# Performance work log

Hardware: AMD Instinct MI355X
Metric: run time of the kernel (lower is better)

## Reference

```python
import jax, jax.numpy as jnp
import numpy as np

N, IN_DIM, OUT_DIM, HEADS = 4096, 256, 256, 8
D_HEAD = (OUT_DIM * HEADS) // HEADS  # = OUT_DIM per the torch code
HIDDEN = OUT_DIM * 4
LN_EPS = 1e-5


def setup_inputs() -> dict:
    key = jax.random.key(0)
    ks = jax.random.split(key, 8)
    s = 0.02
    return {
        "x": jax.random.normal(ks[0], (N, IN_DIM), jnp.float32),
        "Wq": jax.random.normal(ks[1], (OUT_DIM * HEADS, IN_DIM), jnp.float32) * s,
        "Wk": jax.random.normal(ks[2], (OUT_DIM * HEADS, IN_DIM), jnp.float32) * s,
        "Wv": jax.random.normal(ks[3], (OUT_DIM * HEADS, IN_DIM), jnp.float32) * s,
        "Wo": jax.random.normal(ks[4], (OUT_DIM, OUT_DIM * HEADS), jnp.float32) * s,
        "bo": jnp.zeros((OUT_DIM,), jnp.float32),
        "ln1_g": jnp.ones((IN_DIM,), jnp.float32),
        "ln1_b": jnp.zeros((IN_DIM,), jnp.float32),
        "ln2_g": jnp.ones((OUT_DIM,), jnp.float32),
        "ln2_b": jnp.zeros((OUT_DIM,), jnp.float32),
        "W1": jax.random.normal(ks[5], (HIDDEN, OUT_DIM), jnp.float32) * s,
        "b1": jnp.zeros((HIDDEN,), jnp.float32),
        "W2": jax.random.normal(ks[6], (OUT_DIM, HIDDEN), jnp.float32) * s,
        "b2": jnp.zeros((OUT_DIM,), jnp.float32),
    }


def _layernorm(x, g, b):
    mu = jnp.mean(x, axis=-1, keepdims=True)
    var = jnp.mean(jnp.square(x - mu), axis=-1, keepdims=True)
    return (x - mu) * jax.lax.rsqrt(var + LN_EPS) * g + b


def reference(x, Wq, Wk, Wv, Wo, bo, ln1_g, ln1_b, ln2_g, ln2_b, W1, b1, W2, b2):
    n = x.shape[0]
    h = _layernorm(x, ln1_g, ln1_b)
    # projections: F.linear(h, W) = h @ W.T, viewed as [N, H, d_head]
    Q = (h @ Wq.T).reshape(n, HEADS, D_HEAD)
    K = (h @ Wk.T).reshape(n, HEADS, D_HEAD)
    V = (h @ Wv.T).reshape(n, HEADS, D_HEAD)
    scores = jnp.einsum('nhd,mhd->nhm', Q, K) / jnp.sqrt(jnp.float32(D_HEAD))
    probs = jax.nn.softmax(scores, axis=-1)
    attn = jnp.einsum('nhm,mhd->nhd', probs, V).reshape(n, HEADS * D_HEAD)
    attn_out = attn @ Wo.T + bo
    x = x + attn_out  # proj_residual is Identity (in_dim == out_dim)
    h2 = _layernorm(x, ln2_g, ln2_b)
    ffn = jax.nn.gelu(h2 @ W1.T + b1, approximate=False) @ W2.T + b2
    return x + ffn
```

## Files before the change

kernel.cpp:

```cpp
#include <hip/hip_runtime.h>

typedef __attribute__((ext_vector_type(8))) short short8;
typedef __attribute__((ext_vector_type(4))) float f32x4;
typedef __attribute__((ext_vector_type(16))) float f32x16;
typedef __attribute__((ext_vector_type(8))) int i32x8;
typedef unsigned short u16;
typedef unsigned int u32;
typedef unsigned char u8;

#define DEVFN static __device__ __forceinline__

DEVFN u16 f2b(float f) {
  u32 u = __builtin_bit_cast(u32, f);
  u32 r = u + 0x7fffu + ((u >> 16) & 1u);
  return (u16)(r >> 16);
}

DEVFN float b2f(u16 b) {
  u32 u = ((u32)b) << 16;
  return __builtin_bit_cast(float, u);
}

DEVFN short8 ldfrag(const void* p) {
  return __builtin_bit_cast(short8, *(const uint4*)p);
}

#define MFMA16(a, b, c) __builtin_amdgcn_mfma_f32_16x16x32_bf16((a), (b), (c), 0, 0, 0)
#define MFMAS(a, b, c) __builtin_amdgcn_mfma_scale_f32_32x32x64_f8f6f4((a), (b), (c), 0, 0, 0, 127, 0, 127)
#define MFMASW(a, b, c) __builtin_amdgcn_mfma_scale_f32_32x32x64_f8f6f4((a), (b), (c), 0, 0, 0, 127, 0, 123)
#define EXP2(x) __builtin_amdgcn_exp2f(x)
#define CVT8(a, b, o, hi) __builtin_amdgcn_cvt_pk_fp8_f32((a), (b), (o), (hi))

DEVFN i32x8 mk8(uint4 a, uint4 b) {
  return (i32x8){(int)a.x, (int)a.y, (int)a.z, (int)a.w, (int)b.x, (int)b.y, (int)b.z, (int)b.w};
}

DEVFN void llds16(const void* g, void* l) {
  __builtin_amdgcn_global_load_lds((const __attribute__((address_space(1))) void*)g,
                                   (__attribute__((address_space(3))) void*)l, 16, 0, 0);
}

DEVFN float gelu_exact(float v) {
  return 0.5f * v * (1.0f + erff(v * 0.70710678118654752f));
}

DEVFN int sigma(int d) {
  return (d & ~24) | ((d & 8) << 1) | ((d & 16) >> 1);
}

DEVFN size_t c8off(int row, int k) {
  return (size_t)(row >> 5) * 8192 + (k >> 6) * 2048 + ((row & 31) + 32 * ((k >> 5) & 1)) * 32 + (k & 31);
}

__global__ __launch_bounds__(256) void k_prep(const float* Wq, const float* Wk, const float* Wv,
                                              const float* Wo, const float* W1, const float* W2,
                                              u8* Wq8, u8* Wk8, u8* Wv8,
                                              u16* Wob, u8* W18, u16* W2b,
                                              const float* x, const float* g1, const float* be1,
                                              u8* h8c) {
  const int y = blockIdx.y;
  if (y < 3) {
    int i = blockIdx.x * 256 + threadIdx.x;
    if (i >= 131072) return;
    const float* s = y == 0 ? Wq : (y == 1 ? Wk : Wv);
    u8* d = y == 0 ? Wq8 : (y == 1 ? Wk8 : Wv8);
    float4 v = ((const float4*)s)[i];
    const int col = i >> 6, k = (i & 63) * 4;
    u32 q = CVT8(v.x * 16.0f, v.y * 16.0f, 0, false);
    q = CVT8(v.z * 16.0f, v.w * 16.0f, q, true);
    *(u32*)(d + c8off(col, k)) = q;
    return;
  }
  if (y == 4) {
    int i = blockIdx.x * 256 + threadIdx.x;
    if (i >= 65536) return;
    float4 v = ((const float4*)W1)[i];
    const int col = i >> 6, k = (i & 63) * 4;
    u32 q = CVT8(v.x * 16.0f, v.y * 16.0f, 0, false);
    q = CVT8(v.z * 16.0f, v.w * 16.0f, q, true);
    *(u32*)(W18 + c8off(col, k)) = q;
    return;
  }
  if (y < 6) {
    int i = blockIdx.x * 256 + threadIdx.x;
    const float* s = (y == 3) ? Wo : W2;
    u16* d = (y == 3) ? Wob : W2b;
    int n4 = (y == 3) ? 131072 : 65536;
    if (i >= n4) return;
    float4 v = ((const float4*)s)[i];
    ushort4 o = { f2b(v.x), f2b(v.y), f2b(v.z), f2b(v.w) };
    ((ushort4*)d)[i] = o;
    return;
  }
  int row = blockIdx.x * 4 + (threadIdx.x >> 6);
  int l = threadIdx.x & 63;
  const float4 v = *(const float4*)(x + (size_t)row * 256 + l * 4);
  float s = v.x + v.y + v.z + v.w;
#pragma unroll
  for (int m = 1; m < 64; m <<= 1) s += __shfl_xor(s, m);
  float mu = s * (1.0f / 256.0f);
  float dx = v.x - mu, dy = v.y - mu, dz = v.z - mu, dw = v.w - mu;
  float q = dx * dx + dy * dy + dz * dz + dw * dw;
#pragma unroll
  for (int m = 1; m < 64; m <<= 1) q += __shfl_xor(q, m);
  float r = rsqrtf(q * (1.0f / 256.0f) + 1e-5f);
  float4 gv = *(const float4*)(g1 + l * 4);
  float4 bv = *(const float4*)(be1 + l * 4);
  u32 pk = CVT8(dx * r * gv.x + bv.x, dy * r * gv.y + bv.y, 0, false);
  pk = CVT8(dz * r * gv.z + bv.z, dw * r * gv.w + bv.w, pk, true);
  *(u32*)(h8c + c8off(row, l * 4)) = pk;
}

__global__ __launch_bounds__(256, 2) void k_gemm_sk(const u16* __restrict__ A,
                                                    const u16* __restrict__ B,
                                                    u16* __restrict__ out,
                                                    int M, int N, int K) {
  __shared__ __attribute__((aligned(16))) u16 As[128 * 32];
  __shared__ __attribute__((aligned(16))) u16 Bs[128 * 32];
  const int t = threadIdx.x;
  const int w = t >> 6, l = t & 63, g = l >> 4, c = l & 15;
  const int wr = w >> 1, wc = w & 1;
  const int bm = blockIdx.y, bn = blockIdx.x;

  f32x4 acc[4][4] = {};
  int nk = (K >> 5) / gridDim.z, kk0 = blockIdx.z * nk;

  const int srow = t >> 2;
  const int sj = t & 3;
  const char* Abase = (const char*)A;
  const char* Bbase = (const char*)B;

  for (int kk = kk0; kk < kk0 + nk; ++kk) {
    const size_t kb = (size_t)kk * 64;
    uint4 a0 = *(const uint4*)(Abase + ((size_t)(bm * 128 + srow) * K) * 2 + kb + sj * 16);
    uint4 a1 = *(const uint4*)(Abase + ((size_t)(bm * 128 + srow + 64) * K) * 2 + kb + sj * 16);
    uint4 b0 = *(const uint4*)(Bbase + ((size_t)(bn * 128 + srow) * K) * 2 + kb + sj * 16);
    uint4 b1 = *(const uint4*)(Bbase + ((size_t)(bn * 128 + srow + 64) * K) * 2 + kb + sj * 16);
    __syncthreads();
    const int sw0 = (sj * 16) ^ (((srow >> 1) & 3) << 4);
    const int sw1 = (sj * 16) ^ ((((srow + 64) >> 1) & 3) << 4);
    *(uint4*)((char*)As + srow * 64 + sw0) = a0;
    *(uint4*)((char*)As + (srow + 64) * 64 + sw1) = a1;
    *(uint4*)((char*)Bs + srow * 64 + sw0) = b0;
    *(uint4*)((char*)Bs + (srow + 64) * 64 + sw1) = b1;
    __syncthreads();
    short8 af[4], bfr[4];
#pragma unroll
    for (int m = 0; m < 4; ++m) {
      int row = wr * 64 + m * 16 + c;
      af[m] = ldfrag((const char*)As + row * 64 + ((g * 16) ^ (((row >> 1) & 3) << 4)));
    }
#pragma unroll
    for (int n = 0; n < 4; ++n) {
      int row = wc * 64 + n * 16 + c;
      bfr[n] = ldfrag((const char*)Bs + row * 64 + ((g * 16) ^ (((row >> 1) & 3) << 4)));
    }
#pragma unroll
    for (int m = 0; m < 4; ++m)
#pragma unroll
      for (int n = 0; n < 4; ++n) acc[m][n] = MFMA16(af[m], bfr[n], acc[m][n]);
  }

  const int row0 = bm * 128 + wr * 64 + 4 * g;
  const int col0 = bn * 128 + wc * 64 + c;
  u16* po = out + (size_t)blockIdx.z * M * N;
#pragma unroll
  for (int m = 0; m < 4; ++m)
#pragma unroll
    for (int n = 0; n < 4; ++n)
#pragma unroll
      for (int rr = 0; rr < 4; ++rr)
        po[(size_t)(row0 + m * 16 + rr) * N + col0 + n * 16] = f2b(acc[m][n][rr]);
}

__global__ __launch_bounds__(256, 2) void k_gemm_wo(const u16* __restrict__ part,
                                                    const float* __restrict__ ml,
                                                    const u16* __restrict__ B,
                                                    u16* __restrict__ out) {
  constexpr int M = 4096, N = 256, K = 2048;
  __shared__ __attribute__((aligned(16))) u16 As[128 * 32];
  __shared__ __attribute__((aligned(16))) u16 Bs[128 * 32];
  const int t = threadIdx.x;
  const int w = t >> 6, l = t & 63, g = l >> 4, c = l & 15;
  const int wr = w >> 1, wc = w & 1;
  const int bm = blockIdx.y, bn = blockIdx.x;
  const int nk = 16, kk0 = blockIdx.z * 16;
  const int h0 = kk0 >> 3;

  const int srow = t >> 2;
  const int sj = t & 3;
  const int r0 = bm * 128 + srow, r1 = r0 + 64;

  float wgt[4];
#pragma unroll
  for (int rr = 0; rr < 2; ++rr) {
    const int row = rr ? r1 : r0;
#pragma unroll
    for (int hh = 0; hh < 2; ++hh) {
      const int h = h0 + hh;
      float l0 = ml[(0 + h) * 4096 + row];
      float l1 = ml[(8 + h) * 4096 + row];
      wgt[rr * 2 + hh] = 1.0f / (l0 + l1);
    }
  }

  f32x4 acc[4][4] = {};
  const char* Pbase = (const char*)part;
  const char* Bbase = (const char*)B;
  const size_t PSTRIDE = (size_t)4096 * 2048 * 2;

  for (int kk = kk0; kk < kk0 + nk; ++kk) {
    const int hh = (kk >> 3) & 1;
    const size_t kb = (size_t)kk * 64;
    const size_t a0off = ((size_t)r0 * K) * 2 + kb + sj * 16;
    const size_t a1off = ((size_t)r1 * K) * 2 + kb + sj * 16;
    uint4 p00 = *(const uint4*)(Pbase + a0off);
    uint4 p01 = *(const uint4*)(Pbase + PSTRIDE + a0off);
    uint4 p10 = *(const uint4*)(Pbase + a1off);
    uint4 p11 = *(const uint4*)(Pbase + PSTRIDE + a1off);
    uint4 b0 = *(const uint4*)(Bbase + ((size_t)(bn * 128 + srow) * K) * 2 + kb + sj * 16);
    uint4 b1 = *(const uint4*)(Bbase + ((size_t)(bn * 128 + srow + 64) * K) * 2 + kb + sj * 16);

    float w0 = wgt[hh], w1 = wgt[2 + hh];
    uint4 a0, a1;
    {
      const u16* x0 = (const u16*)&p00;
      const u16* x1 = (const u16*)&p01;
      u16* o = (u16*)&a0;
#pragma unroll
      for (int j = 0; j < 8; ++j) o[j] = f2b((b2f(x0[j]) + b2f(x1[j])) * w0);
      const u16* y0 = (const u16*)&p10;
      const u16* y1 = (const u16*)&p11;
      u16* o1 = (u16*)&a1;
#pragma unroll
      for (int j = 0; j < 8; ++j) o1[j] = f2b((b2f(y0[j]) + b2f(y1[j])) * w1);
    }

    __syncthreads();
    const int sw0 = (sj * 16) ^ (((srow >> 1) & 3) << 4);
    const int sw1 = (sj * 16) ^ ((((srow + 64) >> 1) & 3) << 4);
    *(uint4*)((char*)As + srow * 64 + sw0) = a0;
    *(uint4*)((char*)As + (srow + 64) * 64 + sw1) = a1;
    *(uint4*)((char*)Bs + srow * 64 + sw0) = b0;
    *(uint4*)((char*)Bs + (srow + 64) * 64 + sw1) = b1;
    __syncthreads();
    short8 af[4], bfr[4];
#pragma unroll
    for (int m = 0; m < 4; ++m) {
      int row = wr * 64 + m * 16 + c;
      af[m] = ldfrag((const char*)As + row * 64 + ((g * 16) ^ (((row >> 1) & 3) << 4)));
    }
#pragma unroll
    for (int n = 0; n < 4; ++n) {
      int row = wc * 64 + n * 16 + c;
      bfr[n] = ldfrag((const char*)Bs + row * 64 + ((g * 16) ^ (((row >> 1) & 3) << 4)));
    }
#pragma unroll
    for (int m = 0; m < 4; ++m)
#pragma unroll
      for (int n = 0; n < 4; ++n) acc[m][n] = MFMA16(af[m], bfr[n], acc[m][n]);
  }

  const int row0 = bm * 128 + wr * 64 + 4 * g;
  const int col0 = bn * 128 + wc * 64 + c;
  u16* po = out + (size_t)blockIdx.z * M * N;
#pragma unroll
  for (int m = 0; m < 4; ++m)
#pragma unroll
    for (int n = 0; n < 4; ++n)
#pragma unroll
      for (int rr = 0; rr < 4; ++rr)
        po[(size_t)(row0 + m * 16 + rr) * N + col0 + n * 16] = f2b(acc[m][n][rr]);
}

__global__ __launch_bounds__(256, 2) void k_gemm_qkv(const u8* __restrict__ h8c,
                                                     const u8* __restrict__ Wq8,
                                                     const u8* __restrict__ Wk8,
                                                     const u8* __restrict__ Wv8,
                                                     u8* __restrict__ Oq,
                                                     u8* __restrict__ Ok,
                                                     u8* __restrict__ Ov8) {
  __shared__ __attribute__((aligned(16))) char As[32768];
  __shared__ __attribute__((aligned(16))) char Bs[32768];
  const int t = threadIdx.x;
  const int w = t >> 6, l = t & 63;
  const int q31 = l & 31, hi = l >> 5;
  const int wr = w >> 1, wc = w & 1;
  const int sel = blockIdx.x >> 4;
  const int bn = blockIdx.x & 15;
  const int bm = blockIdx.y;
  const u8* B = sel == 0 ? Wq8 : (sel == 1 ? Wk8 : Wv8);

#pragma unroll
  for (int ii = 0; ii < 8; ++ii) {
    const int inst = w * 8 + ii;
    llds16(h8c + (size_t)bm * 32768 + inst * 1024 + l * 16, As + inst * 1024);
  }
#pragma unroll
  for (int ii = 0; ii < 8; ++ii) {
    const int inst = w * 8 + ii;
    llds16(B + (size_t)bn * 32768 + inst * 1024 + l * 16, Bs + inst * 1024);
  }
  asm volatile("s_waitcnt vmcnt(0)" ::: "memory");
  __builtin_amdgcn_s_barrier();

  f32x16 acc[2][2] = {};
#pragma unroll
  for (int ks = 0; ks < 4; ++ks) {
    i32x8 af[2], bf8[2];
#pragma unroll
    for (int m = 0; m < 2; ++m) {
      const char* p = As + ((wr * 2 + m) * 4 + ks) * 2048 + l * 32;
      af[m] = mk8(*(const uint4*)p, *(const uint4*)(p + 16));
    }
#pragma unroll
    for (int n = 0; n < 2; ++n) {
      const char* p = Bs + ((wc * 2 + n) * 4 + ks) * 2048 + l * 32;
      bf8[n] = mk8(*(const uint4*)p, *(const uint4*)(p + 16));
    }
#pragma unroll
    for (int m = 0; m < 2; ++m)
#pragma unroll
      for (int n = 0; n < 2; ++n) acc[m][n] = MFMASW(af[m], bf8[n], acc[m][n]);
  }

#pragma unroll
  for (int m = 0; m < 2; ++m) {
#pragma unroll
    for (int n = 0; n < 2; ++n) {
      const int col = bn * 128 + wc * 64 + n * 32 + q31;
      const int rbase = bm * 128 + wr * 64 + m * 32 + 4 * hi;
      const int d = col & 255, h = col >> 8;
#pragma unroll
      for (int j = 0; j < 4; ++j) {
        const int kv0 = rbase + 8 * j;
        u32 q = CVT8(acc[m][n][4 * j], acc[m][n][4 * j + 1], 0, false);
        q = CVT8(acc[m][n][4 * j + 2], acc[m][n][4 * j + 3], q, true);
        if (sel == 0) {
#pragma unroll
          for (int e = 0; e < 4; ++e)
            Oq[(size_t)(kv0 + e) * 2048 + col] = (u8)(q >> (8 * e));
        } else if (sel == 1) {
#pragma unroll
          for (int e = 0; e < 4; ++e) {
            const int kv = kv0 + e;
            Ok[(size_t)h * 1048576 + (size_t)(kv >> 5) * 8192 + (d >> 6) * 2048 +
               (((d & 31) >> 4)) * 1024 + ((kv & 31) + 32 * ((d >> 5) & 1)) * 16 + (d & 15)] =
                (u8)(q >> (8 * e));
          }
        } else {
          const int s = sigma(kv0 & 31);
          *(u32*)(Ov8 + (size_t)h * 1048576 + (size_t)(kv0 >> 6) * 16384 + (d >> 5) * 2048 +
                  ((kv0 >> 5) & 1) * 1024 + ((d & 31) + 32 * (s >> 4)) * 16 + (s & 15)) = q;
        }
      }
    }
  }
}

__global__ __launch_bounds__(256, 2) void k_gemm_ffn1(const u8* __restrict__ A8,
                                                      const u8* __restrict__ B8,
                                                      const float* __restrict__ bias,
                                                      u16* __restrict__ out) {
  __shared__ __attribute__((aligned(16))) char As[32768];
  __shared__ __attribute__((aligned(16))) char Bs[32768];
  const int t = threadIdx.x;
  const int w = t >> 6, l = t & 63;
  const int q31 = l & 31, hi = l >> 5;
  const int wr = w >> 1, wc = w & 1;
  const int bn = blockIdx.x;
  const int bm = blockIdx.y;

#pragma unroll
  for (int ii = 0; ii < 8; ++ii) {
    const int inst = w * 8 + ii;
    llds16(A8 + (size_t)bm * 32768 + inst * 1024 + l * 16, As + inst * 1024);
  }
#pragma unroll
  for (int ii = 0; ii < 8; ++ii) {
    const int inst = w * 8 + ii;
    llds16(B8 + (size_t)bn * 32768 + inst * 1024 + l * 16, Bs + inst * 1024);
  }
  asm volatile("s_waitcnt vmcnt(0)" ::: "memory");
  __builtin_amdgcn_s_barrier();

  f32x16 acc[2][2] = {};
#pragma unroll
  for (int ks = 0; ks < 4; ++ks) {
    i32x8 af[2], bf8[2];
#pragma unroll
    for (int m = 0; m < 2; ++m) {
      const char* p = As + ((wr * 2 + m) * 4 + ks) * 2048 + l * 32;
      af[m] = mk8(*(const uint4*)p, *(const uint4*)(p + 16));
    }
#pragma unroll
    for (int n = 0; n < 2; ++n) {
      const char* p = Bs + ((wc * 2 + n) * 4 + ks) * 2048 + l * 32;
      bf8[n] = mk8(*(const uint4*)p, *(const uint4*)(p + 16));
    }
#pragma unroll
    for (int m = 0; m < 2; ++m)
#pragma unroll
      for (int n = 0; n < 2; ++n) acc[m][n] = MFMASW(af[m], bf8[n], acc[m][n]);
  }

#pragma unroll
  for (int m = 0; m < 2; ++m) {
#pragma unroll
    for (int n = 0; n < 2; ++n) {
      const int col = bn * 128 + wc * 64 + n * 32 + q31;
      const int rbase = bm * 128 + wr * 64 + m * 32 + 4 * hi;
      const float bc = bias[col];
#pragma unroll
      for (int j = 0; j < 4; ++j) {
        const int r0j = rbase + 8 * j;
#pragma unroll
        for (int e = 0; e < 4; ++e)
          out[(size_t)(r0j + e) * 1024 + col] = f2b(gelu_exact(acc[m][n][4 * j + e] + bc));
      }
    }
  }
}

__global__ __launch_bounds__(256) void k_red4(const u16* __restrict__ p,
                                              const float* __restrict__ bias,
                                              const float* __restrict__ resid,
                                              float* __restrict__ out) {
  int i = blockIdx.x * 256 + threadIdx.x;
  ushort4 a = *(const ushort4*)(p + (size_t)i * 4);
  ushort4 b = *(const ushort4*)(p + 1048576 * 1 + (size_t)i * 4);
  ushort4 c = *(const ushort4*)(p + 1048576 * 2 + (size_t)i * 4);
  ushort4 d = *(const ushort4*)(p + 1048576 * 3 + (size_t)i * 4);
  float4 r = ((const float4*)resid)[i];
  float4 bb = ((const float4*)bias)[i & 63];
  float4 o;
  o.x = b2f(a.x) + b2f(b.x) + b2f(c.x) + b2f(d.x) + r.x + bb.x;
  o.y = b2f(a.y) + b2f(b.y) + b2f(c.y) + b2f(d.y) + r.y + bb.y;
  o.z = b2f(a.z) + b2f(b.z) + b2f(c.z) + b2f(d.z) + r.z + bb.z;
  o.w = b2f(a.w) + b2f(b.w) + b2f(c.w) + b2f(d.w) + r.w + bb.w;
  ((float4*)out)[i] = o;
}

__global__ __launch_bounds__(256) void k_red4ln(const u16* __restrict__ p,
                                                const float* __restrict__ bias,
                                                const float* __restrict__ resid,
                                                const float* __restrict__ g,
                                                const float* __restrict__ b,
                                                float* __restrict__ x2,
                                                u8* __restrict__ h28) {
  int row = blockIdx.x * 4 + (threadIdx.x >> 6);
  int l = threadIdx.x & 63;
  int i = row * 64 + l;
  ushort4 a = *(const ushort4*)(p + (size_t)i * 4);
  ushort4 bq = *(const ushort4*)(p + 1048576 * 1 + (size_t)i * 4);
  ushort4 cq = *(const ushort4*)(p + 1048576 * 2 + (size_t)i * 4);
  ushort4 dq = *(const ushort4*)(p + 1048576 * 3 + (size_t)i * 4);
  float4 r = ((const float4*)resid)[i];
  float4 bi = ((const float4*)bias)[l];
  float4 v;
  v.x = b2f(a.x) + b2f(bq.x) + b2f(cq.x) + b2f(dq.x) + r.x + bi.x;
  v.y = b2f(a.y) + b2f(bq.y) + b2f(cq.y) + b2f(dq.y) + r.y + bi.y;
  v.z = b2f(a.z) + b2f(bq.z) + b2f(cq.z) + b2f(dq.z) + r.z + bi.z;
  v.w = b2f(a.w) + b2f(bq.w) + b2f(cq.w) + b2f(dq.w) + r.w + bi.w;
  ((float4*)x2)[i] = v;
  float s = v.x + v.y + v.z + v.w;
#pragma unroll
  for (int m = 1; m < 64; m <<= 1) s += __shfl_xor(s, m);
  float mu = s * (1.0f / 256.0f);
  float dx = v.x - mu, dy = v.y - mu, dz = v.z - mu, dw = v.w - mu;
  float q = dx * dx + dy * dy + dz * dz + dw * dw;
#pragma unroll
  for (int m = 1; m < 64; m <<= 1) q += __shfl_xor(q, m);
  float rr = rsqrtf(q * (1.0f / 256.0f) + 1e-5f);
  float4 gv = *(const float4*)(g + l * 4);
  float4 bv = *(const float4*)(b + l * 4);
  u32 pk = CVT8(dx * rr * gv.x + bv.x, dy * rr * gv.y + bv.y, 0, false);
  pk = CVT8(dz * rr * gv.z + bv.z, dw * rr * gv.w + bv.w, pk, true);
  *(u32*)(h28 + c8off(row, l * 4)) = pk;
}

__global__ __launch_bounds__(256, 2) void k_attn(const u8* __restrict__ Q8,
                                                 const u8* __restrict__ K8,
                                                 const u8* __restrict__ V8,
                                                 u16* __restrict__ part,
                                                 float* __restrict__ ml) {
  __shared__ __attribute__((aligned(16))) char smem[49152];
  const int t = threadIdx.x;
  const int w = t >> 6, l = t & 63;
  const int q31 = l & 31, hi = l >> 5;
  const int head = blockIdx.x, qb = blockIdx.y, sp = blockIdx.z;
  const int cbase = sp * 64;
  const float C2 = 0.0625f * 1.44269504f;
  const float MC = 16.0f * C2;

  i32x8 qv[4];
  {
    const u8* qp = Q8 + (size_t)(qb * 128 + w * 32 + q31) * 2048 + head * 256 + hi * 32;
#pragma unroll
    for (int m = 0; m < 4; ++m)
      qv[m] = mk8(*(const uint4*)(qp + m * 64), *(const uint4*)(qp + m * 64 + 16));
  }

  f32x16 o[8] = {};
  float lsum = 0.0f;

  const u8* Kc = K8 + (size_t)head * 1048576;
  const u8* Vc = V8 + (size_t)head * 1048576;

  auto stageK = [&](int cc) {
    char* kd = smem + (cc & 1) * 8192;
    const u8* src = Kc + (size_t)(cbase + cc) * 8192;
#pragma unroll
    for (int ii = 0; ii < 2; ++ii) {
      const int inst = w * 2 + ii;
      llds16(src + inst * 1024 + l * 16, kd + inst * 1024);
    }
  };
  auto stageV = [&](int pp) {
    char* vd = smem + 16384 + (pp & 1) * 16384;
    const u8* src = Vc + (size_t)(sp * 32 + pp) * 16384;
#pragma unroll
    for (int ii = 0; ii < 4; ++ii) {
      const int inst = w * 4 + ii;
      llds16(src + inst * 1024 + l * 16, vd + inst * 1024);
    }
  };

  auto qkchunk = [&](int c, u32 pq[4]) {
    const char* kd = smem + (c & 1) * 8192;
    f32x16 s = {};
    __builtin_amdgcn_s_setprio(1);
#pragma unroll
    for (int m = 0; m < 4; ++m) {
      uint4 k0 = *(const uint4*)(kd + m * 2048 + l * 16);
      uint4 k1 = *(const uint4*)(kd + m * 2048 + 1024 + l * 16);
      s = MFMAS(mk8(k0, k1), qv[m], s);
    }
    __builtin_amdgcn_s_setprio(0);
    float p[16];
#pragma unroll
    for (int i = 0; i < 16; ++i) p[i] = EXP2(fmaf(s[i], C2, -MC));
    float r8[8];
#pragma unroll
    for (int i = 0; i < 8; ++i) r8[i] = p[i] + p[i + 8];
#pragma unroll
    for (int i = 0; i < 4; ++i) r8[i] += r8[i + 4];
    float rs = (r8[0] + r8[1]) + (r8[2] + r8[3]);
    rs += __shfl_xor(rs, 32);
    lsum += rs;
    u32 a0 = CVT8(p[0], p[1], 0, false);
    a0 = CVT8(p[2], p[3], a0, true);
    u32 a1 = CVT8(p[4], p[5], 0, false);
    a1 = CVT8(p[6], p[7], a1, true);
    u32 a2 = CVT8(p[8], p[9], 0, false);
    a2 = CVT8(p[10], p[11], a2, true);
    u32 a3 = CVT8(p[12], p[13], 0, false);
    a3 = CVT8(p[14], p[15], a3, true);
    asm("v_permlane32_swap_b32 %0, %1" : "+v"(a0), "+v"(a1));
    asm("v_permlane32_swap_b32 %0, %1" : "+v"(a2), "+v"(a3));
    pq[0] = a0; pq[1] = a1; pq[2] = a2; pq[3] = a3;
  };

  stageK(0);
  stageV(0);
  for (int cp = 0; cp < 32; ++cp) {
    const int c0 = 2 * cp;
    asm volatile("s_waitcnt vmcnt(4)" ::: "memory");
    __builtin_amdgcn_s_barrier();
    __builtin_amdgcn_sched_barrier(0);
    stageK(c0 + 1);
    u32 pe[4];
    qkchunk(c0, pe);

    asm volatile("s_waitcnt vmcnt(0)" ::: "memory");
    __builtin_amdgcn_s_barrier();
    __builtin_amdgcn_sched_barrier(0);
    if (cp < 31) {
      stageK(c0 + 2);
      stageV(cp + 1);
    }
    u32 po[4];
    qkchunk(c0 + 1, po);

    i32x8 a8 = {(int)pe[0], (int)pe[1], (int)pe[2], (int)pe[3],
                (int)po[0], (int)po[1], (int)po[2], (int)po[3]};
    const char* vd = smem + 16384 + (cp & 1) * 16384;
    __builtin_amdgcn_s_setprio(1);
#pragma unroll
    for (int dt = 0; dt < 8; ++dt) {
      uint4 v0 = *(const uint4*)(vd + dt * 2048 + l * 16);
      uint4 v1 = *(const uint4*)(vd + dt * 2048 + 1024 + l * 16);
      o[dt] = MFMAS(a8, mk8(v0, v1), o[dt]);
    }
    __builtin_amdgcn_s_setprio(0);
  }

  u16* pb = part + (size_t)sp * 4096 * 2048;
#pragma unroll
  for (int i = 0; i < 16; ++i) {
    const int r = (i & 3) + 8 * (i >> 2) + 4 * hi;
    const size_t qg = (size_t)(qb * 128 + w * 32 + r);
#pragma unroll
    for (int dt = 0; dt < 8; ++dt)
      pb[qg * 2048 + head * 256 + dt * 32 + q31] = f2b(o[dt][i]);
  }
  if (hi == 0) {
    const int qg = qb * 128 + w * 32 + q31;
    ml[(sp * 8 + head) * 4096 + qg] = lsum;
  }
}

extern "C" void kernel_launch(void* const* d_in, const int* in_sizes, int n_in,
                              void* d_out, int out_size, void* d_ws, size_t ws_size,
                              hipStream_t stream) {
  const float* x   = (const float*)d_in[0];
  const float* Wq  = (const float*)d_in[1];
  const float* Wk  = (const float*)d_in[2];
  const float* Wv  = (const float*)d_in[3];
  const float* Wo  = (const float*)d_in[4];
  const float* bo  = (const float*)d_in[5];
  const float* g1  = (const float*)d_in[6];
  const float* be1 = (const float*)d_in[7];
  const float* g2  = (const float*)d_in[8];
  const float* be2 = (const float*)d_in[9];
  const float* W1  = (const float*)d_in[10];
  const float* b1  = (const float*)d_in[11];
  const float* W2  = (const float*)d_in[12];
  const float* b2  = (const float*)d_in[13];

  char* ws = (char*)d_ws;
  size_t off = 0;
  auto alloc = [&](size_t n) {
    char* p = ws + off;
    off = (off + n + 255) & ~(size_t)255;
    return p;
  };
  u8*  h8c   = (u8*)alloc(4096 * 256);
  u8*  Wq8   = (u8*)alloc(2048 * 256);
  u8*  Wk8   = (u8*)alloc(2048 * 256);
  u8*  Wv8   = (u8*)alloc(2048 * 256);
  u16* Wob   = (u16*)alloc(256 * 2048 * 2);
  u8*  W18   = (u8*)alloc(1024 * 256);
  u16* W2b   = (u16*)alloc(256 * 1024 * 2);
  u8*  Qb8   = (u8*)alloc((size_t)4096 * 2048);
  u8*  Kb8   = (u8*)alloc((size_t)4096 * 2048);
  u8*  Vb8   = (u8*)alloc((size_t)2048 * 4096);
  u16* attnb = (u16*)alloc((size_t)2 * 4096 * 2048 * 2);
  float* mlb = (float*)alloc(16 * 4096 * 4);
  float* x2  = (float*)alloc(4096 * 256 * 4);
  u8*  h28   = (u8*)alloc(4096 * 256);
  u16* ffn1  = (u16*)alloc((size_t)4096 * 1024 * 2);
  u16* pbuf  = (u16*)Qb8;

  k_prep<<<dim3(1024, 7), 256, 0, stream>>>(Wq, Wk, Wv, Wo, W1, W2,
                                            Wq8, Wk8, Wv8, Wob, W18, W2b,
                                            x, g1, be1, h8c);

  k_gemm_qkv<<<dim3(48, 32), 256, 0, stream>>>(h8c, Wq8, Wk8, Wv8, Qb8, Kb8, Vb8);

  k_attn<<<dim3(8, 32, 2), 256, 0, stream>>>(Qb8, Kb8, Vb8, attnb, mlb);

  k_gemm_wo<<<dim3(2, 32, 4), 256, 0, stream>>>(attnb, mlb, Wob, pbuf);
  k_red4ln<<<1024, 256, 0, stream>>>(pbuf, bo, x, g2, be2, x2, h28);
  k_gemm_ffn1<<<dim3(8, 32), 256, 0, stream>>>(h28, W18, b1, ffn1);
  k_gemm_sk<<<dim3(2, 32, 4), 256, 0, stream>>>(ffn1, W2b, pbuf, 4096, 256, 1024);
  k_red4<<<1024, 256, 0, stream>>>(pbuf, b2, x2, (float*)d_out);
}
```

Measured before the change: 144.9 us.

## Quantize FFN hidden activations and W2 to fp8 and use fp8 MFMA for FFN2

```diff
diff --git a/kernel.cpp b/kernel.cpp
--- a/kernel.cpp
+++ b/kernel.cpp
@@ -51,11 +51,14 @@
 DEVFN size_t c8off(int row, int k) {
   return (size_t)(row >> 5) * 8192 + (k >> 6) * 2048 + ((row & 31) + 32 * ((k >> 5) & 1)) * 32 + (k & 31);
 }
+DEVFN size_t c8off1k(int row, int k) {
+  return (size_t)(row >> 5) * 32768 + (k >> 6) * 2048 + ((row & 31) + 32 * ((k >> 5) & 1)) * 32 + (k & 31);
+}
 
 __global__ __launch_bounds__(256) void k_prep(const float* Wq, const float* Wk, const float* Wv,
                                               const float* Wo, const float* W1, const float* W2,
                                               u8* Wq8, u8* Wk8, u8* Wv8,
-                                              u16* Wob, u8* W18, u16* W2b,
+                                              u16* Wob, u8* W18, u8* W28,
                                               const float* x, const float* g1, const float* be1,
                                               u8* h8c) {
   const int y = blockIdx.y;
@@ -81,15 +84,22 @@
     *(u32*)(W18 + c8off(col, k)) = q;
     return;
   }
-  if (y < 6) {
+  if (y == 5) {
     int i = blockIdx.x * 256 + threadIdx.x;
-    const float* s = (y == 3) ? Wo : W2;
-    u16* d = (y == 3) ? Wob : W2b;
-    int n4 = (y == 3) ? 131072 : 65536;
-    if (i >= n4) return;
-    float4 v = ((const float4*)s)[i];
+    if (i >= 65536) return;
+    float4 v = ((const float4*)W2)[i];
+    const int row = i >> 8, k = (i & 255) * 4;
+    u32 q = CVT8(v.x * 16.0f, v.y * 16.0f, 0, false);
+    q = CVT8(v.z * 16.0f, v.w * 16.0f, q, true);
+    *(u32*)(W28 + c8off1k(row, k)) = q;
+    return;
+  }
+  if (y == 3) {
+    int i = blockIdx.x * 256 + threadIdx.x;
+    if (i >= 131072) return;
+    float4 v = ((const float4*)Wo)[i];
     ushort4 o = { f2b(v.x), f2b(v.y), f2b(v.z), f2b(v.w) };
-    ((ushort4*)d)[i] = o;
+    ((ushort4*)Wob)[i] = o;
     return;
   }
   int row = blockIdx.x * 4 + (threadIdx.x >> 6);
@@ -109,68 +119,6 @@
   u32 pk = CVT8(dx * r * gv.x + bv.x, dy * r * gv.y + bv.y, 0, false);
   pk = CVT8(dz * r * gv.z + bv.z, dw * r * gv.w + bv.w, pk, true);
   *(u32*)(h8c + c8off(row, l * 4)) = pk;
-}
-
-__global__ __launch_bounds__(256, 2) void k_gemm_sk(const u16* __restrict__ A,
-                                                    const u16* __restrict__ B,
-                                                    u16* __restrict__ out,
-                                                    int M, int N, int K) {
-  __shared__ __attribute__((aligned(16))) u16 As[128 * 32];
-  __shared__ __attribute__((aligned(16))) u16 Bs[128 * 32];
-  const int t = threadIdx.x;
-  const int w = t >> 6, l = t & 63, g = l >> 4, c = l & 15;
-  const int wr = w >> 1, wc = w & 1;
-  const int bm = blockIdx.y, bn = blockIdx.x;
-
-  f32x4 acc[4][4] = {};
-  int nk = (K >> 5) / gridDim.z, kk0 = blockIdx.z * nk;
-
-  const int srow = t >> 2;
-  const int sj = t & 3;
-  const char* Abase = (const char*)A;
-  const char* Bbase = (const char*)B;
-
-  for (int kk = kk0; kk < kk0 + nk; ++kk) {
-    const size_t kb = (size_t)kk * 64;
-    uint4 a0 = *(const uint4*)(Abase + ((size_t)(bm * 128 + srow) * K) * 2 + kb + sj * 16);
-    uint4 a1 = *(const uint4*)(Abase + ((size_t)(bm * 128 + srow + 64) * K) * 2 + kb + sj * 16);
-    uint4 b0 = *(const uint4*)(Bbase + ((size_t)(bn * 128 + srow) * K) * 2 + kb + sj * 16);
-    uint4 b1 = *(const uint4*)(Bbase + ((size_t)(bn * 128 + srow + 64) * K) * 2 + kb + sj * 16);
-    __syncthreads();
-    const int sw0 = (sj * 16) ^ (((srow >> 1) & 3) << 4);
-    const int sw1 = (sj * 16) ^ ((((srow + 64) >> 1) & 3) << 4);
-    *(uint4*)((char*)As + srow * 64 + sw0) = a0;
-    *(uint4*)((char*)As + (srow + 64) * 64 + sw1) = a1;
-    *(uint4*)((char*)Bs + srow * 64 + sw0) = b0;
-    *(uint4*)((char*)Bs + (srow + 64) * 64 + sw1) = b1;
-    __syncthreads();
-    short8 af[4], bfr[4];
-#pragma unroll
-    for (int m = 0; m < 4; ++m) {
-      int row = wr * 64 + m * 16 + c;
-      af[m] = ldfrag((const char*)As + row * 64 + ((g * 16) ^ (((row >> 1) & 3) << 4)));
-    }
-#pragma unroll
-    for (int n = 0; n < 4; ++n) {
-      int row = wc * 64 + n * 16 + c;
-      bfr[n] = ldfrag((const char*)Bs + row * 64 + ((g * 16) ^ (((row >> 1) & 3) << 4)));
-    }
-#pragma unroll
-    for (int m = 0; m < 4; ++m)
-#pragma unroll
-      for (int n = 0; n < 4; ++n) acc[m][n] = MFMA16(af[m], bfr[n], acc[m][n]);
-  }
-
-  const int row0 = bm * 128 + wr * 64 + 4 * g;
-  const int col0 = bn * 128 + wc * 64 + c;
-  u16* po = out + (size_t)blockIdx.z * M * N;
-#pragma unroll
-  for (int m = 0; m < 4; ++m)
-#pragma unroll
-    for (int n = 0; n < 4; ++n)
-#pragma unroll
-      for (int rr = 0; rr < 4; ++rr)
-        po[(size_t)(row0 + m * 16 + rr) * N + col0 + n * 16] = f2b(acc[m][n][rr]);
 }
 
 __global__ __launch_bounds__(256, 2) void k_gemm_wo(const u16* __restrict__ part,
@@ -361,6 +309,72 @@
 __global__ __launch_bounds__(256, 2) void k_gemm_ffn1(const u8* __restrict__ A8,
                                                       const u8* __restrict__ B8,
                                                       const float* __restrict__ bias,
+                                                      u8* __restrict__ out8) {
+  __shared__ __attribute__((aligned(16))) char As[32768];
+  __shared__ __attribute__((aligned(16))) char Bs[32768];
+  const int t = threadIdx.x;
+  const int w = t >> 6, l = t & 63;
+  const int q31 = l & 31, hi = l >> 5;
+  const int wr = w >> 1, wc = w & 1;
+  const int bn = blockIdx.x;
+  const int bm = blockIdx.y;
+
+#pragma unroll
+  for (int ii = 0; ii < 8; ++ii) {
+    const int inst = w * 8 + ii;
+    llds16(A8 + (size_t)bm * 32768 + inst * 1024 + l * 16, As + inst * 1024);
+  }
+#pragma unroll
+  for (int ii = 0; ii < 8; ++ii) {
+    const int inst = w * 8 + ii;
+    llds16(B8 + (size_t)bn * 32768 + inst * 1024 + l * 16, Bs + inst * 1024);
+  }
+  asm volatile("s_waitcnt vmcnt(0)" ::: "memory");
+  __builtin_amdgcn_s_barrier();
+
+  f32x16 acc[2][2] = {};
+#pragma unroll
+  for (int ks = 0; ks < 4; ++ks) {
+    i32x8 af[2], bf8[2];
+#pragma unroll
+    for (int m = 0; m < 2; ++m) {
+      const char* p = As + ((wr * 2 + m) * 4 + ks) * 2048 + l * 32;
+      af[m] = mk8(*(const uint4*)p, *(const uint4*)(p + 16));
+    }
+#pragma unroll
+    for (int n = 0; n < 2; ++n) {
+      const char* p = Bs + ((wc * 2 + n) * 4 + ks) * 2048 + l * 32;
+      bf8[n] = mk8(*(const uint4*)p, *(const uint4*)(p + 16));
+    }
+#pragma unroll
+    for (int m = 0; m < 2; ++m)
+#pragma unroll
+      for (int n = 0; n < 2; ++n) acc[m][n] = MFMASW(af[m], bf8[n], acc[m][n]);
+  }
+
+#pragma unroll
+  for (int m = 0; m < 2; ++m) {
+#pragma unroll
+    for (int n = 0; n < 2; ++n) {
+      const int col = bn * 128 + wc * 64 + n * 32 + q31;
+      const int rbase = bm * 128 + wr * 64 + m * 32 + 4 * hi;
+      const float bc = bias[col];
+      const size_t base = (size_t)(rbase >> 5) * 32768 + (col >> 6) * 2048 +
+                          32 * ((col >> 5) & 1) * 32 + (col & 31);
+#pragma unroll
+      for (int j = 0; j < 4; ++j) {
+        const int rl = (rbase & 31) + 8 * j;
+#pragma unroll
+        for (int e = 0; e < 4; ++e)
+          out8[base + (size_t)(rl + e) * 32] =
+              (u8)(CVT8(gelu_exact(acc[m][n][4 * j + e] + bc), 0.0f, 0, false) & 0xff);
+      }
+    }
+  }
+}
+
+__global__ __launch_bounds__(256, 2) void k_gemm_ffn2(const u8* __restrict__ A8,
+                                                      const u8* __restrict__ B8,
                                                       u16* __restrict__ out) {
   __shared__ __attribute__((aligned(16))) char As[32768];
   __shared__ __attribute__((aligned(16))) char Bs[32768];
@@ -370,16 +384,19 @@
   const int wr = w >> 1, wc = w & 1;
   const int bn = blockIdx.x;
   const int bm = blockIdx.y;
+  const int z = blockIdx.z;
 
 #pragma unroll
   for (int ii = 0; ii < 8; ++ii) {
     const int inst = w * 8 + ii;
-    llds16(A8 + (size_t)bm * 32768 + inst * 1024 + l * 16, As + inst * 1024);
+    llds16(A8 + (size_t)(bm * 4 + (inst >> 3)) * 32768 + z * 8192 + (inst & 7) * 1024 + l * 16,
+           As + inst * 1024);
   }
 #pragma unroll
   for (int ii = 0; ii < 8; ++ii) {
     const int inst = w * 8 + ii;
-    llds16(B8 + (size_t)bn * 32768 + inst * 1024 + l * 16, Bs + inst * 1024);
+    llds16(B8 + (size_t)(bn * 4 + (inst >> 3)) * 32768 + z * 8192 + (inst & 7) * 1024 + l * 16,
+           Bs + inst * 1024);
   }
   asm volatile("s_waitcnt vmcnt(0)" ::: "memory");
   __builtin_amdgcn_s_barrier();
@@ -404,19 +421,19 @@
       for (int n = 0; n < 2; ++n) acc[m][n] = MFMASW(af[m], bf8[n], acc[m][n]);
   }
 
+  u16* po = out + (size_t)z * 4096 * 256;
 #pragma unroll
   for (int m = 0; m < 2; ++m) {
 #pragma unroll
     for (int n = 0; n < 2; ++n) {
       const int col = bn * 128 + wc * 64 + n * 32 + q31;
       const int rbase = bm * 128 + wr * 64 + m * 32 + 4 * hi;
-      const float bc = bias[col];
 #pragma unroll
       for (int j = 0; j < 4; ++j) {
         const int r0j = rbase + 8 * j;
 #pragma unroll
         for (int e = 0; e < 4; ++e)
-          out[(size_t)(r0j + e) * 1024 + col] = f2b(gelu_exact(acc[m][n][4 * j + e] + bc));
+          po[(size_t)(r0j + e) * 256 + col] = f2b(acc[m][n][4 * j + e]);
       }
     }
   }
@@ -641,7 +658,7 @@
   u8*  Wv8   = (u8*)alloc(2048 * 256);
   u16* Wob   = (u16*)alloc(256 * 2048 * 2);
   u8*  W18   = (u8*)alloc(1024 * 256);
-  u16* W2b   = (u16*)alloc(256 * 1024 * 2);
+  u8*  W28   = (u8*)alloc(256 * 1024);
   u8*  Qb8   = (u8*)alloc((size_t)4096 * 2048);
   u8*  Kb8   = (u8*)alloc((size_t)4096 * 2048);
   u8*  Vb8   = (u8*)alloc((size_t)2048 * 4096);
@@ -649,11 +666,11 @@
   float* mlb = (float*)alloc(16 * 4096 * 4);
   float* x2  = (float*)alloc(4096 * 256 * 4);
   u8*  h28   = (u8*)alloc(4096 * 256);
-  u16* ffn1  = (u16*)alloc((size_t)4096 * 1024 * 2);
+  u8*  ffn18 = (u8*)alloc((size_t)4096 * 1024);
   u16* pbuf  = (u16*)Qb8;
 
   k_prep<<<dim3(1024, 7), 256, 0, stream>>>(Wq, Wk, Wv, Wo, W1, W2,
-                                            Wq8, Wk8, Wv8, Wob, W18, W2b,
+                                            Wq8, Wk8, Wv8, Wob, W18, W28,
                                             x, g1, be1, h8c);
 
   k_gemm_qkv<<<dim3(48, 32), 256, 0, stream>>>(h8c, Wq8, Wk8, Wv8, Qb8, Kb8, Vb8);
@@ -662,7 +679,7 @@
 
   k_gemm_wo<<<dim3(2, 32, 4), 256, 0, stream>>>(attnb, mlb, Wob, pbuf);
   k_red4ln<<<1024, 256, 0, stream>>>(pbuf, bo, x, g2, be2, x2, h28);
-  k_gemm_ffn1<<<dim3(8, 32), 256, 0, stream>>>(h28, W18, b1, ffn1);
-  k_gemm_sk<<<dim3(2, 32, 4), 256, 0, stream>>>(ffn1, W2b, pbuf, 4096, 256, 1024);
+  k_gemm_ffn1<<<dim3(8, 32), 256, 0, stream>>>(h28, W18, b1, ffn18);
+  k_gemm_ffn2<<<dim3(2, 32, 4), 256, 0, stream>>>(ffn18, W28, pbuf);
   k_red4<<<1024, 256, 0, stream>>>(pbuf, b2, x2, (float*)d_out);
 }
```

Result: faster. 141.9 us (-2.1%).
